# Kernel optimization log

Measured on AMD Instinct MI355X. Metric: run time of the kernel, lower is better.

The kernel has to match this reference:

```python
import jax, jax.numpy as jnp
import numpy as np

B, M, D = 2048, 40, 64          # batch, num fields, embedding dim
HIDDEN = [128, 128, 128]        # CIN layer sizes


def setup_inputs() -> dict:
    key = jax.random.key(0)
    kx, k0, k1, k2 = jax.random.split(key, 4)
    x = jax.random.normal(kx, (B, M, D), dtype=jnp.float32)
    # torch.rand -> uniform [0, 1)
    W0 = jax.random.uniform(k0, (M, M, HIDDEN[0]), dtype=jnp.float32)
    W1 = jax.random.uniform(k1, (M, HIDDEN[0], HIDDEN[1]), dtype=jnp.float32)
    W2 = jax.random.uniform(k2, (M, HIDDEN[1], HIDDEN[2]), dtype=jnp.float32)
    return {"x": x, "W0": W0, "W1": W1, "W2": W2}


def _cin_forward(x, Ws):
    # x: [b, m, d]. Each layer k:
    #   x_next[b, l, d] = sum_{m, h} x0[b, m, d] * x_k[b, h, d] * W_k[m, h, l]
    # which equals the torch 'bil,bjl->bjil' outer product followed by
    # 'bijk,ijl->bkl' + transpose, but expressed as one fused contraction
    # (opt_einsum picks a path avoiding the worst intermediate).
    ps = []
    xk = x  # [b, H_k, d], H_0 = m
    for W in Ws:
        x_next = jnp.einsum('bmd,bhd,mhl->bld', x, xk, W)  # [b, L_k, d]
        ps.append(jnp.sum(x_next, axis=2))                  # [b, L_k]
        xk = x_next
    return jnp.concatenate(ps, axis=1)                      # [b, sum(L_k)]


def reference(x, W0, W1, W2):
    return _cin_forward(x, (W0, W1, W2))
```

## Files before the change

kernel.cpp:

```cpp
#include <hip/hip_runtime.h>
#include <hip/hip_bf16.h>
#include <cstdint>

#define BATCH 2048
#define MF    40
#define DDIM  64
#define LDIM  128
#define ROWS  (BATCH * DDIM)

typedef __attribute__((ext_vector_type(4)))  short    short4_t;
typedef __attribute__((ext_vector_type(8)))  short    short8;
typedef __attribute__((ext_vector_type(8)))  __bf16   bf16x8;
typedef __attribute__((ext_vector_type(16))) float    floatx16;
typedef __attribute__((ext_vector_type(4)))  uint32_t uint4_t;

__device__ __forceinline__ unsigned short f32_to_bf16(float f) {
    union { float f; uint32_t u; } v; v.f = f;
    uint32_t u = v.u;
    uint32_t r = (u + 0x7fffu + ((u >> 16) & 1u)) >> 16;
    return (unsigned short)r;
}

__device__ __forceinline__ uint32_t scale2(uint32_t w, float s) {
    float lo = __builtin_bit_cast(float, w << 16);
    float hi = __builtin_bit_cast(float, w & 0xffff0000u);
    uint32_t plo = __builtin_bit_cast(uint32_t, lo * s) + 0x8000u;
    uint32_t phi = __builtin_bit_cast(uint32_t, hi * s) + 0x8000u;
    return __builtin_amdgcn_perm(phi, plo, 0x07060302u);
}

__device__ __forceinline__ bf16x8 scale_frag(bf16x8 a, float s) {
    uint4_t w = __builtin_bit_cast(uint4_t, a);
    uint4_t r;
#pragma unroll
    for (int i = 0; i < 4; ++i) r[i] = scale2(w[i], s);
    return __builtin_bit_cast(bf16x8, r);
}

__global__ void k_wprep(const float* __restrict__ W, unsigned short* __restrict__ Wt,
                        int KK, int H) {
    int bi = blockIdx.x;
    int lane = threadIdx.x;
    int cb = bi & 3;
    int mkk = bi >> 2;
    int kk = mkk % KK, m = mkk / KK;
    int l = cb * 32 + (lane & 31);
    int hbase = kk * 16 + (lane >> 5) * 8;
    unsigned short o[8];
#pragma unroll
    for (int j = 0; j < 8; ++j) {
        int h = hbase + j;
        float v = (h < H) ? W[((size_t)m * H + h) * LDIM + l] : 0.f;
        o[j] = f32_to_bf16(v);
    }
    *(short8*)(Wt + ((size_t)bi * 64 + lane) * 8) = *(const short8*)o;
}

template <int KK, bool FIRST, int OFF, bool WRITEX>
__global__ __launch_bounds__(256, 2) void k_gemm(
    const float* __restrict__ x,
    const unsigned short* __restrict__ Xprev,
    const unsigned short* __restrict__ Wt,
    unsigned short* __restrict__ Xout,
    float* __restrict__ out)
{
    __shared__ unsigned short slab[2][KK * 2048];

    const int tid  = threadIdx.x;
    const int lane = tid & 63, wave = tid >> 6;
    const int hf   = lane >> 5, r31 = lane & 31;
    const int b = blockIdx.x * 4 + wave;

    bf16x8 afrag[2][KK];
    if constexpr (FIRST) {
#pragma unroll
        for (int t = 0; t < 2; ++t)
#pragma unroll
            for (int kk = 0; kk < KK; ++kk) {
                unsigned short tmp[8];
#pragma unroll
                for (int j = 0; j < 8; ++j) {
                    int h = kk * 16 + hf * 8 + j;
                    float v = (h < MF) ? x[((size_t)b * MF + h) * DDIM + t * 32 + r31] : 0.f;
                    tmp[j] = f32_to_bf16(v);
                }
                afrag[t][kk] = __builtin_bit_cast(bf16x8, *(const short8*)tmp);
            }
    } else {
        const int g = r31 >> 3, hs = (r31 >> 2) & 1, ii = r31 & 3;
#pragma unroll
        for (int t = 0; t < 2; ++t) {
            int tile = b * 2 + t;
#pragma unroll
            for (int kk = 0; kk < KK; ++kk) {
                int k0  = kk * 16 + hf * 8;
                int cbk = k0 >> 5, rr = k0 & 31;
                const unsigned short* p =
                    Xprev + ((size_t)(((tile * 4 + cbk) * 4 + g) * 2 + hs) * 32 + rr) * 4 + ii;
                unsigned short tmp[8];
#pragma unroll
                for (int j = 0; j < 8; ++j) tmp[j] = p[(size_t)j * 4];
                afrag[t][kk] = __builtin_bit_cast(bf16x8, *(const short8*)tmp);
            }
        }
    }

    floatx16 acc[2][4] = {};

    auto stage = [&](int m, int buf) {
        const unsigned short* src = Wt + (size_t)m * (KK * 2048);
#pragma unroll
        for (int it = 0; it < KK; ++it) {
            int c = it * 256 + tid;
            __builtin_amdgcn_global_load_lds(
                (const __attribute__((address_space(1))) uint32_t*)(src + (size_t)c * 8),
                (__attribute__((address_space(3))) uint32_t*)(&slab[buf][(size_t)c * 8]),
                16, 0, 0);
        }
    };

    auto ldfrag = [&](const unsigned short* sl, int kk, int cb) {
        return __builtin_bit_cast(
            bf16x8, *(const short8*)(sl + ((size_t)(kk * 4 + cb) * 64 + lane) * 8));
    };

    const float* sb = x + (size_t)b * MF * DDIM + r31;
    float s0 = sb[0], s1 = sb[32];
    float sn0, sn1;

    constexpr int NS = 2 * KK;

    stage(0, 0);
#pragma unroll 1
    for (int m = 0; m < MF; ++m) {
        asm volatile("s_waitcnt vmcnt(0)" ::: "memory");
        __syncthreads();
        int mn = (m + 1 < MF) ? m + 1 : m;
        sn0 = sb[(size_t)mn * DDIM];
        sn1 = sb[(size_t)mn * DDIM + 32];
        if (m + 1 < MF) stage(m + 1, (m + 1) & 1);

        const unsigned short* sl = slab[m & 1];

        bf16x8 bbuf[2][2];
#pragma unroll
        for (int p = 0; p < 2; ++p) {
            bbuf[p][0] = ldfrag(sl, 0, p * 2 + 0);
            bbuf[p][1] = ldfrag(sl, 0, p * 2 + 1);
        }

        bf16x8 z0, z1;
#pragma unroll
        for (int s = 0; s < NS; ++s) {
            const int kk = s >> 1, pr = s & 1, slot = s & 1;
            if (pr == 0) {
                z0 = scale_frag(afrag[0][kk], s0);
                z1 = scale_frag(afrag[1][kk], s1);
            }
            acc[0][pr * 2 + 0] = __builtin_amdgcn_mfma_f32_32x32x16_bf16(z0, bbuf[slot][0], acc[0][pr * 2 + 0], 0, 0, 0);
            acc[1][pr * 2 + 0] = __builtin_amdgcn_mfma_f32_32x32x16_bf16(z1, bbuf[slot][0], acc[1][pr * 2 + 0], 0, 0, 0);
            acc[0][pr * 2 + 1] = __builtin_amdgcn_mfma_f32_32x32x16_bf16(z0, bbuf[slot][1], acc[0][pr * 2 + 1], 0, 0, 0);
            acc[1][pr * 2 + 1] = __builtin_amdgcn_mfma_f32_32x32x16_bf16(z1, bbuf[slot][1], acc[1][pr * 2 + 1], 0, 0, 0);
            if (s + 2 < NS) {
                const int kn = (s + 2) >> 1, prn = (s + 2) & 1;
                bbuf[slot][0] = ldfrag(sl, kn, prn * 2 + 0);
                bbuf[slot][1] = ldfrag(sl, kn, prn * 2 + 1);
            }
        }
        s0 = sn0; s1 = sn1;
    }

    if constexpr (WRITEX) {
#pragma unroll
        for (int t = 0; t < 2; ++t) {
            int tile = b * 2 + t;
#pragma unroll
            for (int cb = 0; cb < 4; ++cb) {
#pragma unroll
                for (int g = 0; g < 4; ++g) {
                    unsigned short o[4];
#pragma unroll
                    for (int i = 0; i < 4; ++i) o[i] = f32_to_bf16(acc[t][cb][g * 4 + i]);
                    *(short4_t*)(Xout +
                        ((size_t)(((tile * 4 + cb) * 4 + g) * 2 + hf) * 32 + r31) * 4) =
                        *(const short4_t*)o;
                }
            }
        }
    }

#pragma unroll
    for (int cb = 0; cb < 4; ++cb) {
        float v = 0.f;
#pragma unroll
        for (int j = 0; j < 16; ++j) v += acc[0][cb][j] + acc[1][cb][j];
        v += __shfl_xor(v, 32);
        if (hf == 0)
            out[(size_t)b * 384 + OFF + cb * 32 + r31] = v;
    }
}

extern "C" void kernel_launch(void* const* d_in, const int* in_sizes, int n_in,
                              void* d_out, int out_size, void* d_ws, size_t ws_size,
                              hipStream_t stream) {
    const float* x  = (const float*)d_in[0];
    const float* W0 = (const float*)d_in[1];
    const float* W1 = (const float*)d_in[2];
    const float* W2 = (const float*)d_in[3];
    float* out = (float*)d_out;

    char* ws = (char*)d_ws;
    size_t off = 0;
    auto alloc = [&](size_t bytes) -> void* {
        void* p = ws + off;
        off += (bytes + 255) & ~(size_t)255;
        return p;
    };
    unsigned short* W0t = (unsigned short*)alloc((size_t)MF * 3 * 2048 * 2);
    unsigned short* W1t = (unsigned short*)alloc((size_t)MF * 8 * 2048 * 2);
    unsigned short* W2t = (unsigned short*)alloc((size_t)MF * 8 * 2048 * 2);
    unsigned short* X1p = (unsigned short*)alloc((size_t)ROWS * LDIM * 2);
    unsigned short* X2p = (unsigned short*)alloc((size_t)ROWS * LDIM * 2);

    k_wprep<<<MF * 3 * 4, 64, 0, stream>>>(W0, W0t, 3, 40);
    k_wprep<<<MF * 8 * 4, 64, 0, stream>>>(W1, W1t, 8, 128);
    k_wprep<<<MF * 8 * 4, 64, 0, stream>>>(W2, W2t, 8, 128);

    k_gemm<3, true,  0,   true ><<<ROWS / 256, 256, 0, stream>>>(x, nullptr, W0t, X1p, out);
    k_gemm<8, false, 128, true ><<<ROWS / 256, 256, 0, stream>>>(x, X1p,     W1t, X2p, out);
    k_gemm<8, false, 256, false><<<ROWS / 256, 256, 0, stream>>>(x, X2p,     W2t, X2p, out);
}
```

Before: 492.0 us.

## Load weight fragments directly from global memory instead of LDS double-buffer

Removes the LDS staging of the per-field weight slab and the per-iteration barrier. Each wave now loads its B fragments straight from global memory (L2/cache shared across the 4 waves and across blocks) and prefetches across the m-loop boundary. The intent is to drop __syncthreads and the vmcnt(0) waits. The cost is that every wave issues its own global loads with higher latency and only a two-deep register prefetch.

```diff
diff --git a/kernel.cpp b/kernel.cpp
--- a/kernel.cpp
+++ b/kernel.cpp
@@ -64,8 +64,6 @@
     unsigned short* __restrict__ Xout,
     float* __restrict__ out)
 {
-    __shared__ unsigned short slab[2][KK * 2048];
-
     const int tid  = threadIdx.x;
     const int lane = tid & 63, wave = tid >> 6;
     const int hf   = lane >> 5, r31 = lane & 31;
@@ -107,47 +105,28 @@
 
     floatx16 acc[2][4] = {};
 
-    auto stage = [&](int m, int buf) {
-        const unsigned short* src = Wt + (size_t)m * (KK * 2048);
-#pragma unroll
-        for (int it = 0; it < KK; ++it) {
-            int c = it * 256 + tid;
-            __builtin_amdgcn_global_load_lds(
-                (const __attribute__((address_space(1))) uint32_t*)(src + (size_t)c * 8),
-                (__attribute__((address_space(3))) uint32_t*)(&slab[buf][(size_t)c * 8]),
-                16, 0, 0);
-        }
-    };
-
-    auto ldfrag = [&](const unsigned short* sl, int kk, int cb) {
+    auto ldg = [&](int flat_kk, int cb) {
         return __builtin_bit_cast(
-            bf16x8, *(const short8*)(sl + ((size_t)(kk * 4 + cb) * 64 + lane) * 8));
+            bf16x8, *(const short8*)(Wt + (((size_t)flat_kk * 4 + cb) * 64 + lane) * 8));
     };
 
     const float* sb = x + (size_t)b * MF * DDIM + r31;
     float s0 = sb[0], s1 = sb[32];
-    float sn0, sn1;
 
     constexpr int NS = 2 * KK;
 
-    stage(0, 0);
+    bf16x8 bbuf[2][2];
+#pragma unroll
+    for (int p = 0; p < 2; ++p) {
+        bbuf[p][0] = ldg(0, p * 2 + 0);
+        bbuf[p][1] = ldg(0, p * 2 + 1);
+    }
+
 #pragma unroll 1
     for (int m = 0; m < MF; ++m) {
-        asm volatile("s_waitcnt vmcnt(0)" ::: "memory");
-        __syncthreads();
-        int mn = (m + 1 < MF) ? m + 1 : m;
-        sn0 = sb[(size_t)mn * DDIM];
-        sn1 = sb[(size_t)mn * DDIM + 32];
-        if (m + 1 < MF) stage(m + 1, (m + 1) & 1);
-
-        const unsigned short* sl = slab[m & 1];
-
-        bf16x8 bbuf[2][2];
-#pragma unroll
-        for (int p = 0; p < 2; ++p) {
-            bbuf[p][0] = ldfrag(sl, 0, p * 2 + 0);
-            bbuf[p][1] = ldfrag(sl, 0, p * 2 + 1);
-        }
+        const int mn = (m + 1 < MF) ? m + 1 : m;
+        float snn0 = sb[(size_t)mn * DDIM];
+        float snn1 = sb[(size_t)mn * DDIM + 32];
 
         bf16x8 z0, z1;
 #pragma unroll
@@ -161,13 +140,17 @@
             acc[1][pr * 2 + 0] = __builtin_amdgcn_mfma_f32_32x32x16_bf16(z1, bbuf[slot][0], acc[1][pr * 2 + 0], 0, 0, 0);
             acc[0][pr * 2 + 1] = __builtin_amdgcn_mfma_f32_32x32x16_bf16(z0, bbuf[slot][1], acc[0][pr * 2 + 1], 0, 0, 0);
             acc[1][pr * 2 + 1] = __builtin_amdgcn_mfma_f32_32x32x16_bf16(z1, bbuf[slot][1], acc[1][pr * 2 + 1], 0, 0, 0);
-            if (s + 2 < NS) {
-                const int kn = (s + 2) >> 1, prn = (s + 2) & 1;
-                bbuf[slot][0] = ldfrag(sl, kn, prn * 2 + 0);
-                bbuf[slot][1] = ldfrag(sl, kn, prn * 2 + 1);
+            {
+                const int sn = s + 2;
+                int kkn, prn, mb;
+                if (sn < NS) { kkn = sn >> 1;        prn = sn & 1;        mb = m;  }
+                else         { kkn = (sn - NS) >> 1; prn = (sn - NS) & 1; mb = mn; }
+                const int flat = mb * KK + kkn;
+                bbuf[slot][0] = ldg(flat, prn * 2 + 0);
+                bbuf[slot][1] = ldg(flat, prn * 2 + 1);
             }
         }
-        s0 = sn0; s1 = sn1;
+        s0 = snn0; s1 = snn1;
     }
 
     if constexpr (WRITEX) {
```

After: 925.4 us. 1.88x slower.
